# Performance work log

Measured on AMD Instinct MI355X. Metric: run time of the kernel, lower is better.

## Reference

```python
import jax, jax.numpy as jnp
import numpy as np

N, E, G = 50000, 400000, 2000
H, HEADS, HD = 128, 4, 32


def setup_inputs() -> dict:
    key = jax.random.key(0)
    ks = jax.random.split(key, 16)
    nrm = lambda k, shape, s=0.05: jax.random.normal(k, shape, dtype=jnp.float32) * s
    inp = {}
    inp["x"] = jax.random.normal(ks[0], (N, 39), dtype=jnp.float32)
    inp["edge_index"] = jax.random.randint(ks[1], (2, E), 0, N, dtype=jnp.int32)
    inp["edge_attr"] = jax.random.normal(ks[2], (E, 8), dtype=jnp.float32)
    inp["batch"] = jnp.sort(jax.random.randint(ks[3], (N,), 0, G, dtype=jnp.int32))
    inp["in_W"] = nrm(ks[4], (39, H)); inp["in_b"] = jnp.zeros((H,), jnp.float32)
    inp["in_g"] = jnp.ones((H,), jnp.float32); inp["in_beta"] = jnp.zeros((H,), jnp.float32)
    inp["Wl"] = nrm(ks[5], (3, H, H)); inp["Wr"] = nrm(ks[6], (3, H, H))
    inp["We"] = nrm(ks[7], (3, 8, H)); inp["att"] = nrm(ks[8], (3, HEADS, HD))
    inp["conv_b"] = jnp.zeros((3, H), jnp.float32)
    inp["bn_g"] = jnp.ones((3, H), jnp.float32); inp["bn_b"] = jnp.zeros((3, H), jnp.float32)
    inp["t1_W"] = nrm(ks[9], (3 * H, 256)); inp["t1_b"] = jnp.zeros((256,), jnp.float32)
    inp["t1_g"] = jnp.ones((256,), jnp.float32); inp["t1_beta"] = jnp.zeros((256,), jnp.float32)
    inp["t2_W"] = nrm(ks[10], (256, 128)); inp["t2_b"] = jnp.zeros((128,), jnp.float32)
    inp["t2_g"] = jnp.ones((128,), jnp.float32); inp["t2_beta"] = jnp.zeros((128,), jnp.float32)
    inp["head_W"] = nrm(ks[11], (128, 12)); inp["head_b"] = jnp.zeros((12,), jnp.float32)
    return inp


def _bn(h, g, b):
    # BatchNorm1d in training mode: normalize with batch statistics.
    m = h.mean(0)
    v = ((h - m) ** 2).mean(0)
    return g * (h - m) * jax.lax.rsqrt(v + 1e-5) + b


def reference(x, edge_index, edge_attr, batch, in_W, in_b, in_g, in_beta,
              Wl, Wr, We, att, conv_b, bn_g, bn_b,
              t1_W, t1_b, t1_g, t1_beta, t2_W, t2_b, t2_g, t2_beta,
              head_W, head_b):
    src, dst = edge_index[0], edge_index[1]  # messages flow src -> dst (PyG convention)
    xn = jax.nn.relu(_bn(x @ in_W + in_b, in_g, in_beta))  # [N, H]
    for l in range(3):  # three residual GATv2 layers
        xl = (xn @ Wl[l]).reshape(N, HEADS, HD)  # lin_l (source transform)
        xr = (xn @ Wr[l]).reshape(N, HEADS, HD)  # lin_r (target transform)
        ep = (edge_attr @ We[l]).reshape(E, HEADS, HD)
        m = jax.nn.leaky_relu(xl[src] + xr[dst] + ep, 0.2)  # [E, HEADS, HD]
        alpha = jnp.einsum('ehd,hd->eh', m, att[l])  # [E, HEADS]
        amax = jax.ops.segment_max(alpha, dst, num_segments=N)
        amax = jnp.where(jnp.isfinite(amax), amax, 0.0)  # nodes with no in-edges
        ae = jnp.exp(alpha - amax[dst])
        denom = jax.ops.segment_sum(ae, dst, num_segments=N)
        a = ae / (denom[dst] + 1e-16)  # scatter-softmax over neighborhoods
        agg = jax.ops.segment_sum(xl[src] * a[:, :, None], dst, num_segments=N)
        h = agg.reshape(N, H) + conv_b[l]
        h = jax.nn.elu(_bn(h, bn_g[l], bn_b[l]))
        xn = xn + h
    # 3-way global pooling per graph
    cnt = jax.ops.segment_sum(jnp.ones((N,), jnp.float32), batch, num_segments=G)
    sadd = jax.ops.segment_sum(xn, batch, num_segments=G)
    smean = sadd / jnp.maximum(cnt, 1.0)[:, None]
    smax = jax.ops.segment_max(xn, batch, num_segments=G)
    smax = jnp.where(cnt[:, None] > 0, smax, 0.0)
    xg = jnp.concatenate([smean, smax, sadd], axis=1)  # [G, 3H]
    t = jax.nn.relu(_bn(xg @ t1_W + t1_b, t1_g, t1_beta))
    t = jax.nn.relu(_bn(t @ t2_W + t2_b, t2_g, t2_beta))
    return jax.nn.sigmoid(t @ head_W + head_b)  # [G, 12]
```

## Files before the change

### kernel.cpp

```cpp
#include <hip/hip_runtime.h>
#include <math.h>


constexpr int N_ = 50000;
constexpr int E_ = 400000;
constexpr int G_ = 2000;
constexpr int H_ = 128;
constexpr int IN_ = 39;

typedef __attribute__((ext_vector_type(8))) short bf16x8;
typedef __attribute__((ext_vector_type(4))) float f32x4;

__device__ __forceinline__ unsigned pk_bf16(float a, float b) {
  unsigned ua = __float_as_uint(a);
  unsigned ub = __float_as_uint(b);
  ua = (ua + 0x7fffu + ((ua >> 16) & 1u)) >> 16;
  ub = (ub + 0x7fffu + ((ub >> 16) & 1u)) & 0xffff0000u;
  return ua | ub;
}
__device__ __forceinline__ unsigned short bf16_1(float x) {
  unsigned u = __float_as_uint(x);
  u = (u + 0x7fffu + ((u >> 16) & 1u)) >> 16;
  return (unsigned short)u;
}
__device__ __forceinline__ float up_lo(unsigned u) { return __uint_as_float(u << 16); }
__device__ __forceinline__ float up_hi(unsigned u) { return __uint_as_float(u & 0xffff0000u); }

template <int CTRL>
__device__ __forceinline__ float dpp_radd(float x) {
  int y = __builtin_amdgcn_update_dpp(0, __float_as_int(x), CTRL, 0xF, 0xF, false);
  return x + __int_as_float(y);
}
__device__ __forceinline__ float row_reduce16(float p) {
  p = dpp_radd<0x121>(p);
  p = dpp_radd<0x122>(p);
  p = dpp_radd<0x124>(p);
  p = dpp_radd<0x128>(p);
  return p;
}

__global__ __launch_bounds__(256) void hist_kernel(const int* __restrict__ keys, int n,
                                                   int* __restrict__ cnt) {
  for (int i = blockIdx.x * 256 + threadIdx.x; i < n; i += gridDim.x * 256)
    atomicAdd(&cnt[keys[i]], 1);
}

__global__ __launch_bounds__(1024) void scan_local(const int* __restrict__ in,
                                                   int* __restrict__ outx,
                                                   int* __restrict__ bsum, int n) {
  __shared__ int wsum[16];
  int t = threadIdx.x, lane = t & 63, wid = t >> 6;
  int idx = blockIdx.x * 1024 + t;
  int v = (idx < n) ? in[idx] : 0;
  int x = v;
#pragma unroll
  for (int off = 1; off < 64; off <<= 1) {
    int y = __shfl_up(x, off, 64);
    if (lane >= off) x += y;
  }
  if (lane == 63) wsum[wid] = x;
  __syncthreads();
  if (t == 0) {
    int acc = 0;
#pragma unroll
    for (int w = 0; w < 16; w++) { int tmp = wsum[w]; wsum[w] = acc; acc += tmp; }
    bsum[blockIdx.x] = acc;
  }
  __syncthreads();
  if (idx < n) outx[idx] = wsum[wid] + x - v;
}

__global__ __launch_bounds__(64) void scan_bsum(const int* __restrict__ bsum,
                                                int* __restrict__ boff, int nb) {
  int t = threadIdx.x;
  int v = (t < nb) ? bsum[t] : 0;
  int x = v;
#pragma unroll
  for (int off = 1; off < 64; off <<= 1) {
    int y = __shfl_up(x, off, 64);
    if (t >= off) x += y;
  }
  boff[t] = x - v;
}

__global__ __launch_bounds__(1024) void scan_add(int* __restrict__ eoff,
                                                 const int* __restrict__ boff,
                                                 int* __restrict__ cursor, int n) {
  int idx = blockIdx.x * 1024 + threadIdx.x;
  if (idx < n) {
    int e = eoff[idx] + boff[idx >> 10];
    eoff[idx] = e;
    cursor[idx] = e;
  }
  if (idx == 0) eoff[n] = E_;
}

__global__ __launch_bounds__(256) void goff_from_sorted(const int* __restrict__ batch,
                                                        int* __restrict__ goff) {
  int i = blockIdx.x * 256 + threadIdx.x;
  if (i >= N_) return;
  int bi = batch[i];
  int bp = (i == 0) ? -1 : batch[i - 1];
  for (int g = bp + 1; g <= bi; g++) goff[g] = i;
  if (i == N_ - 1) {
    for (int g = bi + 1; g <= G_; g++) goff[g] = N_;
  }
}

__global__ __launch_bounds__(256) void edge_scatter(const int* __restrict__ ei,
                                                    const float* __restrict__ ea,
                                                    int* __restrict__ cursor,
                                                    int* __restrict__ esrc,
                                                    unsigned* __restrict__ easb) {
  int e = blockIdx.x * 256 + threadIdx.x;
  if (e >= E_) return;
  int src = ei[e];
  int dst = ei[E_ + e];
  int j = atomicAdd(&cursor[dst], 1);
  esrc[j] = src;
  const float4* eav = (const float4*)(ea + (size_t)e * 8);
  float4 a0 = eav[0], a1 = eav[1];
  uint4 o;
  o.x = pk_bf16(a0.x, a0.y);
  o.y = pk_bf16(a0.z, a0.w);
  o.z = pk_bf16(a1.x, a1.y);
  o.w = pk_bf16(a1.z, a1.w);
  ((uint4*)easb)[j] = o;
}

__global__ __launch_bounds__(256) void pack_weights(const float* __restrict__ Wl,
                                                    const float* __restrict__ Wr,
                                                    unsigned short* __restrict__ wpack) {
  int i = blockIdx.x * 256 + threadIdx.x;
  if (i >= 3 * 128 * 256) return;
  int l = i >> 15;
  int rem = i & 32767;
  int k = rem >> 8;
  int n = rem & 255;
  const float* Wsrc = (n < 128) ? (Wl + l * H_ * H_) : (Wr + l * H_ * H_);
  int nn = n & 127;
  wpack[(size_t)l * 32768 + n * 128 + k] = bf16_1(Wsrc[k * H_ + nn]);
}

__global__ __launch_bounds__(256) void in_gemm(const float* __restrict__ x,
                                               const float* __restrict__ W,
                                               const float* __restrict__ b,
                                               float* __restrict__ y,
                                               float* __restrict__ ssum,
                                               float* __restrict__ ssq) {
  __shared__ float xs[32][40];
  __shared__ float s1[256], s2[256];
  int t = threadIdx.x;
  int row0 = blockIdx.x * 32;
  for (int i = t; i < 32 * IN_; i += 256) {
    int r = i / IN_, k = i % IN_;
    int row = row0 + r;
    xs[r][k] = (row < N_) ? x[row * IN_ + k] : 0.f;
  }
  __syncthreads();
  int col = t & 127;
  int half = t >> 7;
  float acc[16];
#pragma unroll
  for (int r = 0; r < 16; r++) acc[r] = 0.f;
  for (int k = 0; k < IN_; k++) {
    float w = W[k * H_ + col];
#pragma unroll
    for (int r = 0; r < 16; r++) acc[r] = fmaf(xs[half * 16 + r][k], w, acc[r]);
  }
  float bb = b[col];
  float a1 = 0.f, a2 = 0.f;
#pragma unroll
  for (int r = 0; r < 16; r++) {
    int row = row0 + half * 16 + r;
    float v = acc[r] + bb;
    if (row < N_) {
      y[row * H_ + col] = v;
      a1 += v;
      a2 = fmaf(v, v, a2);
    }
  }
  s1[t] = a1; s2[t] = a2;
  __syncthreads();
  if (t < 128) {
    atomicAdd(&ssum[t], s1[t] + s1[t + 128]);
    atomicAdd(&ssq[t], s2[t] + s2[t + 128]);
  }
}

template <int MODE>
__global__ __launch_bounds__(256) void gemm_mfma(float* __restrict__ xn,
                                                 const float* __restrict__ buf,
                                                 const float* __restrict__ g,
                                                 const float* __restrict__ beta,
                                                 const float* __restrict__ ssum,
                                                 const float* __restrict__ ssq,
                                                 float rows_inv,
                                                 const unsigned short* __restrict__ wp,
                                                 unsigned* __restrict__ xlb,
                                                 unsigned* __restrict__ xrb) {
  __shared__ char smem[17408 + 20480];
  short (*a_s)[136] = (short(*)[136])smem;
  short (*b_s)[40] = (short(*)[40])(smem + 17408);
  float* t2base = (float*)(smem + 17408);
  int t = threadIdx.x;
  int lane = t & 63, w = t >> 6;
  int quad = lane >> 4, lc = lane & 15;
  int row0 = blockIdx.x * 64;

  {
    int r = t >> 2;
    int row = row0 + r;
    int kb0 = (t & 3) * 32;
    bool valid = row < N_;
    for (int kk = 0; kk < 32; kk += 4) {
      int c = kb0 + kk;
      float4 v = make_float4(0.f, 0.f, 0.f, 0.f);
      if (valid) {
        float4 bv = *(const float4*)&buf[(size_t)row * H_ + c];
        float4 gv = *(const float4*)&g[c];
        float4 be = *(const float4*)&beta[c];
        float4 s1 = *(const float4*)&ssum[c];
        float4 s2 = *(const float4*)&ssq[c];
        float m0 = s1.x * rows_inv, m1 = s1.y * rows_inv, m2 = s1.z * rows_inv, m3 = s1.w * rows_inv;
        float r0 = rsqrtf(s2.x * rows_inv - m0 * m0 + 1e-5f);
        float r1 = rsqrtf(s2.y * rows_inv - m1 * m1 + 1e-5f);
        float r2 = rsqrtf(s2.z * rows_inv - m2 * m2 + 1e-5f);
        float r3 = rsqrtf(s2.w * rows_inv - m3 * m3 + 1e-5f);
        float t0 = gv.x * (bv.x - m0) * r0 + be.x;
        float t1 = gv.y * (bv.y - m1) * r1 + be.y;
        float t2 = gv.z * (bv.z - m2) * r2 + be.z;
        float t3 = gv.w * (bv.w - m3) * r3 + be.w;
        if (MODE == 1) {
          v = make_float4(fmaxf(t0, 0.f), fmaxf(t1, 0.f), fmaxf(t2, 0.f), fmaxf(t3, 0.f));
        } else {
          float4 xo = *(const float4*)&xn[(size_t)row * H_ + c];
          v.x = xo.x + ((t0 > 0.f) ? t0 : (__expf(t0) - 1.f));
          v.y = xo.y + ((t1 > 0.f) ? t1 : (__expf(t1) - 1.f));
          v.z = xo.z + ((t2 > 0.f) ? t2 : (__expf(t2) - 1.f));
          v.w = xo.w + ((t3 > 0.f) ? t3 : (__expf(t3) - 1.f));
        }
        *(float4*)&xn[(size_t)row * H_ + c] = v;
      }
      uint2 pk;
      pk.x = pk_bf16(v.x, v.y);
      pk.y = pk_bf16(v.z, v.w);
      *(uint2*)&a_s[r][c] = pk;
    }
  }

  f32x4 acc[16];
#pragma unroll
  for (int nt = 0; nt < 16; nt++) acc[nt] = (f32x4){0.f, 0.f, 0.f, 0.f};

  for (int kb = 0; kb < 4; kb++) {
    __syncthreads();
    for (int i = t; i < 1024; i += 256) {
      int n = i >> 2;
      int k8 = (i & 3) * 8;
      *(uint4*)&b_s[n][k8] = *(const uint4*)&wp[(size_t)n * 128 + kb * 32 + k8];
    }
    __syncthreads();
    bf16x8 av = *(const bf16x8*)&a_s[w * 16 + lc][kb * 32 + quad * 8];
#pragma unroll
    for (int nt = 0; nt < 16; nt++) {
      bf16x8 bv = *(const bf16x8*)&b_s[nt * 16 + lc][quad * 8];
      acc[nt] = __builtin_amdgcn_mfma_f32_16x16x32_bf16(av, bv, acc[nt], 0, 0, 0);
    }
  }
  __syncthreads();

  float* t2 = t2base + w * 544;
  for (int ntp = 0; ntp < 8; ntp++) {
#pragma unroll
    for (int rr = 0; rr < 4; rr++) {
      t2[(quad * 4 + rr) * 34 + lc] = acc[2 * ntp][rr];
      t2[(quad * 4 + rr) * 34 + 16 + lc] = acc[2 * ntp + 1][rr];
    }
    __asm__ volatile("s_waitcnt lgkmcnt(0)" ::: "memory");
#pragma unroll
    for (int it = 0; it < 4; it++) {
      int item = lane + it * 64;
      int p = item & 15, rowi = item >> 4;
      float v0 = t2[rowi * 34 + 2 * p];
      float v1 = t2[rowi * 34 + 2 * p + 1];
      unsigned u = pk_bf16(v0, v1);
      int colpair = ntp * 16 + p;
      int rowg = row0 + w * 16 + rowi;
      if (rowg < N_) {
        if (colpair < 64) xlb[(size_t)rowg * 64 + colpair] = u;
        else xrb[(size_t)rowg * 64 + colpair - 64] = u;
      }
    }
    __asm__ volatile("s_waitcnt lgkmcnt(0)" ::: "memory");
  }
}

__device__ __forceinline__ float ep8u(const uint4& u, const float* w) {
  float ep = up_lo(u.x) * w[0];
  ep = fmaf(up_hi(u.x), w[1], ep);
  ep = fmaf(up_lo(u.y), w[2], ep);
  ep = fmaf(up_hi(u.y), w[3], ep);
  ep = fmaf(up_lo(u.z), w[4], ep);
  ep = fmaf(up_hi(u.z), w[5], ep);
  ep = fmaf(up_lo(u.w), w[6], ep);
  ep = fmaf(up_hi(u.w), w[7], ep);
  return ep;
}

template <bool MASK>
__device__ __forceinline__ void pack4(int spre, int j, int cnt, int base, int l,
                                      const unsigned* __restrict__ xlb,
                                      const uint4* __restrict__ eas4,
                                      float xr0, float xr1,
                                      const float* w0, const float* w1,
                                      float2 attv,
                                      float& acc0, float& acc1, float& den) {
  int i0 = j;
  int i1 = j + 1, i2 = j + 2, i3 = j + 3;
  if (MASK) {
    i1 = (i1 < cnt) ? i1 : cnt - 1;
    i2 = (i2 < cnt) ? i2 : cnt - 1;
    i3 = (i3 < cnt) ? i3 : cnt - 1;
  }
  int s0 = __builtin_amdgcn_readlane(spre, i0);
  int s1 = __builtin_amdgcn_readlane(spre, i1);
  int s2 = __builtin_amdgcn_readlane(spre, i2);
  int s3 = __builtin_amdgcn_readlane(spre, i3);
  unsigned xu0 = xlb[(size_t)s0 * 64 + l];
  unsigned xu1 = xlb[(size_t)s1 * 64 + l];
  unsigned xu2 = xlb[(size_t)s2 * 64 + l];
  unsigned xu3 = xlb[(size_t)s3 * 64 + l];
  uint4 u0 = eas4[base + i0];
  uint4 u1 = eas4[base + i1];
  uint4 u2 = eas4[base + i2];
  uint4 u3 = eas4[base + i3];
  float x00 = up_lo(xu0), x01 = up_hi(xu0);
  float x10 = up_lo(xu1), x11 = up_hi(xu1);
  float x20 = up_lo(xu2), x21 = up_hi(xu2);
  float x30 = up_lo(xu3), x31 = up_hi(xu3);
  float m00 = x00 + xr0 + ep8u(u0, w0);
  float m01 = x01 + xr1 + ep8u(u0, w1);
  float m10 = x10 + xr0 + ep8u(u1, w0);
  float m11 = x11 + xr1 + ep8u(u1, w1);
  float m20 = x20 + xr0 + ep8u(u2, w0);
  float m21 = x21 + xr1 + ep8u(u2, w1);
  float m30 = x30 + xr0 + ep8u(u3, w0);
  float m31 = x31 + xr1 + ep8u(u3, w1);
  m00 = (m00 > 0.f) ? m00 : 0.2f * m00;
  m01 = (m01 > 0.f) ? m01 : 0.2f * m01;
  m10 = (m10 > 0.f) ? m10 : 0.2f * m10;
  m11 = (m11 > 0.f) ? m11 : 0.2f * m11;
  m20 = (m20 > 0.f) ? m20 : 0.2f * m20;
  m21 = (m21 > 0.f) ? m21 : 0.2f * m21;
  m30 = (m30 > 0.f) ? m30 : 0.2f * m30;
  m31 = (m31 > 0.f) ? m31 : 0.2f * m31;
  float p0 = fmaf(m00, attv.x, m01 * attv.y);
  float p1 = fmaf(m10, attv.x, m11 * attv.y);
  float p2 = fmaf(m20, attv.x, m21 * attv.y);
  float p3 = fmaf(m30, attv.x, m31 * attv.y);
  p0 = row_reduce16(p0);
  p1 = row_reduce16(p1);
  p2 = row_reduce16(p2);
  p3 = row_reduce16(p3);
  float e0v = __expf(p0), e1v = __expf(p1), e2v = __expf(p2), e3v = __expf(p3);
  if (MASK) {
    if (j + 1 >= cnt) e1v = 0.f;
    if (j + 2 >= cnt) e2v = 0.f;
    if (j + 3 >= cnt) e3v = 0.f;
  }
  acc0 = fmaf(e0v, x00, acc0); acc1 = fmaf(e0v, x01, acc1);
  acc0 = fmaf(e1v, x10, acc0); acc1 = fmaf(e1v, x11, acc1);
  acc0 = fmaf(e2v, x20, acc0); acc1 = fmaf(e2v, x21, acc1);
  acc0 = fmaf(e3v, x30, acc0); acc1 = fmaf(e3v, x31, acc1);
  den += (e0v + e1v) + (e2v + e3v);
}

__global__ __launch_bounds__(256) void agg_csr(const int* __restrict__ eoff,
                                               const int* __restrict__ esrc,
                                               const unsigned* __restrict__ easb,
                                               const float* __restrict__ Wel,
                                               const float* __restrict__ attl,
                                               const unsigned* __restrict__ xlb,
                                               const unsigned* __restrict__ xrb,
                                               const float* __restrict__ cb,
                                               float* __restrict__ buf,
                                               float* __restrict__ ssum,
                                               float* __restrict__ ssq) {
  __shared__ float sA[256], sB[256], sC[256], sD[256];
  int t = threadIdx.x;
  int l = t & 63;
  int sub = t >> 6;
  int c0 = l * 2;
  float w0[8], w1[8];
#pragma unroll
  for (int k = 0; k < 8; k++) {
    float2 wv = *(const float2*)&Wel[k * H_ + c0];
    w0[k] = wv.x; w1[k] = wv.y;
  }
  float2 attv = *(const float2*)&attl[c0];
  float2 cbv = *(const float2*)&cb[c0];
  const uint4* eas4 = (const uint4*)easb;
  float a1_0 = 0.f, a1_1 = 0.f, a2_0 = 0.f, a2_1 = 0.f;
  for (int n = blockIdx.x * 4 + sub; n < N_; n += gridDim.x * 4) {
    unsigned xru = xrb[(size_t)n * 64 + l];
    float xr0 = up_lo(xru), xr1 = up_hi(xru);
    int e0 = eoff[n], e1 = eoff[n + 1];
    float acc0 = 0.f, acc1 = 0.f, den = 0.f;
    for (int base = e0; base < e1; base += 64) {
      int cnt = min(64, e1 - base);
      int spre = (base + l < e1) ? esrc[base + l] : 0;
      int j = 0;
      for (; j + 4 <= cnt; j += 4)
        pack4<false>(spre, j, cnt, base, l, xlb, eas4, xr0, xr1, w0, w1, attv,
                     acc0, acc1, den);
      if (j < cnt)
        pack4<true>(spre, j, cnt, base, l, xlb, eas4, xr0, xr1, w0, w1, attv,
                    acc0, acc1, den);
    }
    float inv = 1.f / (den + 1e-16f);
    float h0 = acc0 * inv + cbv.x;
    float h1 = acc1 * inv + cbv.y;
    *(float2*)&buf[(size_t)n * H_ + c0] = make_float2(h0, h1);
    a1_0 += h0; a1_1 += h1;
    a2_0 = fmaf(h0, h0, a2_0); a2_1 = fmaf(h1, h1, a2_1);
  }
  sA[t] = a1_0; sB[t] = a1_1; sC[t] = a2_0; sD[t] = a2_1;
  __syncthreads();
  if (t < 64) {
    float r1 = sA[t] + sA[t + 64] + sA[t + 128] + sA[t + 192];
    float r2 = sB[t] + sB[t + 64] + sB[t + 128] + sB[t + 192];
    float r3 = sC[t] + sC[t + 64] + sC[t + 128] + sC[t + 192];
    float r4 = sD[t] + sD[t + 64] + sD[t + 128] + sD[t + 192];
    atomicAdd(&ssum[2 * t], r1);
    atomicAdd(&ssum[2 * t + 1], r2);
    atomicAdd(&ssq[2 * t], r3);
    atomicAdd(&ssq[2 * t + 1], r4);
  }
}

__global__ __launch_bounds__(256) void apply_bn_relu(const float* __restrict__ y,
                                                     float* __restrict__ out,
                                                     const float* __restrict__ g,
                                                     const float* __restrict__ beta,
                                                     const float* __restrict__ ssum,
                                                     const float* __restrict__ ssq,
                                                     float rows_inv,
                                                     long total, int cmask) {
  long i = (long)blockIdx.x * 256 + threadIdx.x;
  if (i >= total) return;
  int c = (int)i & cmask;
  float m = ssum[c] * rows_inv;
  float rs = rsqrtf(ssq[c] * rows_inv - m * m + 1e-5f);
  float v = g[c] * (y[i] - m) * rs + beta[c];
  out[i] = fmaxf(v, 0.f);
}

__global__ __launch_bounds__(128) void pool_residual(const int* __restrict__ goff,
                                                     const float* __restrict__ xn,
                                                     const float* __restrict__ buf,
                                                     const float* __restrict__ g,
                                                     const float* __restrict__ beta,
                                                     const float* __restrict__ ssum,
                                                     const float* __restrict__ ssq,
                                                     float rows_inv,
                                                     float* __restrict__ xg) {
  int gr = blockIdx.x;
  int t = threadIdx.x;
  int n0 = goff[gr], n1 = goff[gr + 1];
  float mm = ssum[t] * rows_inv;
  float rr = rsqrtf(ssq[t] * rows_inv - mm * mm + 1e-5f);
  float gg = g[t], bb = beta[t];
  float s = 0.f, mx = -INFINITY;
  for (int n = n0; n < n1; n++) {
    float w = gg * (buf[(size_t)n * H_ + t] - mm) * rr + bb;
    w = (w > 0.f) ? w : (__expf(w) - 1.f);
    float v = xn[(size_t)n * H_ + t] + w;
    s += v;
    mx = fmaxf(mx, v);
  }
  float c = (float)(n1 - n0);
  xg[gr * 384 + t] = s / fmaxf(c, 1.f);
  xg[gr * 384 + 128 + t] = (c > 0.f) ? mx : 0.f;
  xg[gr * 384 + 256 + t] = s;
}

template <int K, int COLS>
__global__ void mlp_gemm(const float* __restrict__ A, const float* __restrict__ W,
                         const float* __restrict__ b, float* __restrict__ Y, int rows,
                         float* __restrict__ ssum, float* __restrict__ ssq) {
  __shared__ float xs[8][K];
  int t = threadIdx.x;
  int row0 = blockIdx.x * 8;
  for (int i = t; i < 8 * K; i += COLS) {
    int r = i / K, k = i % K;
    int row = row0 + r;
    xs[r][k] = (row < rows) ? A[row * K + k] : 0.f;
  }
  __syncthreads();
  float acc[8];
#pragma unroll
  for (int r = 0; r < 8; r++) acc[r] = 0.f;
  for (int k = 0; k < K; k++) {
    float w = W[k * COLS + t];
#pragma unroll
    for (int r = 0; r < 8; r++) acc[r] = fmaf(xs[r][k], w, acc[r]);
  }
  float bb = b[t];
  float a1 = 0.f, a2 = 0.f;
#pragma unroll
  for (int r = 0; r < 8; r++) {
    int row = row0 + r;
    if (row < rows) {
      float v = acc[r] + bb;
      Y[row * COLS + t] = v;
      a1 += v;
      a2 = fmaf(v, v, a2);
    }
  }
  atomicAdd(&ssum[t], a1);
  atomicAdd(&ssq[t], a2);
}

__global__ __launch_bounds__(64) void head_kernel(const float* __restrict__ u,
                                                  const float* __restrict__ W,
                                                  const float* __restrict__ b,
                                                  float* __restrict__ out) {
  __shared__ float row[128];
  int g = blockIdx.x;
  int t = threadIdx.x;
  row[t] = u[g * 128 + t];
  row[t + 64] = u[g * 128 + 64 + t];
  __syncthreads();
  if (t < 12) {
    float acc = b[t];
    for (int k = 0; k < 128; k++) acc = fmaf(row[k], W[k * 12 + t], acc);
    out[g * 12 + t] = 1.f / (1.f + expf(-acc));
  }
}

extern "C" void kernel_launch(void* const* d_in, const int* in_sizes, int n_in, void* d_out,
                              int out_size, void* d_ws, size_t ws_size, hipStream_t stream) {
  (void)in_sizes; (void)n_in; (void)out_size; (void)ws_size;
  const float* x       = (const float*)d_in[0];
  const int*   ei      = (const int*)d_in[1];
  const float* ea      = (const float*)d_in[2];
  const int*   batch   = (const int*)d_in[3];
  const float* in_W    = (const float*)d_in[4];
  const float* in_b    = (const float*)d_in[5];
  const float* in_g    = (const float*)d_in[6];
  const float* in_beta = (const float*)d_in[7];
  const float* Wl      = (const float*)d_in[8];
  const float* Wr      = (const float*)d_in[9];
  const float* We      = (const float*)d_in[10];
  const float* att     = (const float*)d_in[11];
  const float* conv_b  = (const float*)d_in[12];
  const float* bn_g    = (const float*)d_in[13];
  const float* bn_b    = (const float*)d_in[14];
  const float* t1_W    = (const float*)d_in[15];
  const float* t1_b    = (const float*)d_in[16];
  const float* t1_g    = (const float*)d_in[17];
  const float* t1_beta = (const float*)d_in[18];
  const float* t2_W    = (const float*)d_in[19];
  const float* t2_b    = (const float*)d_in[20];
  const float* t2_g    = (const float*)d_in[21];
  const float* t2_beta = (const float*)d_in[22];
  const float* head_W  = (const float*)d_in[23];
  const float* head_b  = (const float*)d_in[24];
  float* out = (float*)d_out;

  float* p = (float*)d_ws;
  float* xn    = p; p += N_ * H_;
  float* buf   = p; p += N_ * H_;
  float* sstat = p; p += 6 * 512;
  float* xg    = p; p += G_ * 384;
  float* u1    = p; p += G_ * 256;
  float* u2    = p; p += G_ * 128;
  unsigned* up = (unsigned*)p;
  unsigned* xlb  = up; up += (size_t)N_ * 64;
  unsigned* xrb  = up; up += (size_t)N_ * 64;
  unsigned* easb = up; up += (size_t)E_ * 4;
  unsigned short* wpack = (unsigned short*)up; up += 3 * 32768 / 2;
  int* ip = (int*)up;
  int* deg    = ip; ip += N_;
  int* eoff   = ip; ip += N_ + 1;
  int* cursor = ip; ip += N_;
  int* goff   = ip; ip += G_ + 1;
  int* esrc   = ip; ip += E_;
  int* bsum   = ip; ip += 64;
  int* boff   = ip; ip += 64;

#define SSUM(s) (sstat + (s) * 512)
#define SSQ(s)  (sstat + (s) * 512 + 256)

  hipMemsetAsync(deg, 0, (size_t)N_ * sizeof(int), stream);
  hipMemsetAsync(sstat, 0, 6 * 512 * sizeof(float), stream);
  hist_kernel<<<1024, 256, 0, stream>>>(ei + E_, E_, deg);
  scan_local<<<49, 1024, 0, stream>>>(deg, eoff, bsum, N_);
  scan_bsum<<<1, 64, 0, stream>>>(bsum, boff, 49);
  scan_add<<<49, 1024, 0, stream>>>(eoff, boff, cursor, N_);
  edge_scatter<<<(E_ + 255) / 256, 256, 0, stream>>>(ei, ea, cursor, esrc, easb);
  goff_from_sorted<<<(N_ + 255) / 256, 256, 0, stream>>>(batch, goff);
  pack_weights<<<384, 256, 0, stream>>>(Wl, Wr, wpack);

  in_gemm<<<(N_ + 31) / 32, 256, 0, stream>>>(x, in_W, in_b, buf, SSUM(0), SSQ(0));

  const float rnInv = 1.f / N_;
  for (int l = 0; l < 3; l++) {
    if (l == 0) {
      gemm_mfma<1><<<782, 256, 0, stream>>>(xn, buf, in_g, in_beta, SSUM(0), SSQ(0), rnInv,
                                            wpack + (size_t)l * 32768, xlb, xrb);
    } else {
      gemm_mfma<2><<<782, 256, 0, stream>>>(xn, buf, bn_g + (l - 1) * H_, bn_b + (l - 1) * H_,
                                            SSUM(l), SSQ(l), rnInv,
                                            wpack + (size_t)l * 32768, xlb, xrb);
    }
    agg_csr<<<2048, 256, 0, stream>>>(eoff, esrc, easb, We + l * 8 * H_, att + l * H_,
                                      xlb, xrb, conv_b + l * H_, buf, SSUM(l + 1), SSQ(l + 1));
  }

  pool_residual<<<G_, 128, 0, stream>>>(goff, xn, buf, bn_g + 2 * H_, bn_b + 2 * H_,
                                        SSUM(3), SSQ(3), rnInv, xg);

  const float rgInv = 1.f / G_;
  mlp_gemm<384, 256><<<G_ / 8, 256, 0, stream>>>(xg, t1_W, t1_b, u1, G_, SSUM(4), SSQ(4));
  apply_bn_relu<<<(G_ * 256 + 255) / 256, 256, 0, stream>>>(u1, u1, t1_g, t1_beta,
                                                            SSUM(4), SSQ(4), rgInv,
                                                            (long)G_ * 256, 255);

  mlp_gemm<256, 128><<<G_ / 8, 128, 0, stream>>>(u1, t2_W, t2_b, u2, G_, SSUM(5), SSQ(5));
  apply_bn_relu<<<(G_ * 128 + 255) / 256, 256, 0, stream>>>(u2, u2, t2_g, t2_beta,
                                                            SSUM(5), SSQ(5), rgInv,
                                                            (long)G_ * 128, 127);

  head_kernel<<<G_, 64, 0, stream>>>(u2, head_W, head_b, out);
#undef SSUM
#undef SSQ
}
```

Baseline: 852.2 us.

## Process node pairs per wave with LDS-staged edge attrs and prefetched gathers

The CSR aggregation kernel now handles two consecutive destination nodes per wavefront. When their combined in-degree fits in 64, it stages the edge attributes in LDS and software-pipelines the gathers of source features one 4-edge pack ahead. The goal is to amortize per-node setup, cut partially filled 64-edge chunks for low-degree nodes, and hide gather latency. It costs extra branching and registers, and pairs whose combined degree exceeds 64 fall back to the old per-node path.

```diff
diff --git a/kernel.cpp b/kernel.cpp
--- a/kernel.cpp
+++ b/kernel.cpp
@@ -376,6 +376,25 @@
   den += (e0v + e1v) + (e2v + e3v);
 }
 
+__device__ __forceinline__ void solo_node(int e0, int e1, int l,
+                                          const int* __restrict__ esrc,
+                                          const unsigned* __restrict__ xlb,
+                                          const uint4* __restrict__ eas4,
+                                          float xr0, float xr1,
+                                          const float* w0, const float* w1,
+                                          float2 attv,
+                                          float& acc0, float& acc1, float& den) {
+  for (int base = e0; base < e1; base += 64) {
+    int cnt = min(64, e1 - base);
+    int spre = (base + l < e1) ? esrc[base + l] : 0;
+    int j = 0;
+    for (; j + 4 <= cnt; j += 4)
+      pack4<false>(spre, j, cnt, base, l, xlb, eas4, xr0, xr1, w0, w1, attv, acc0, acc1, den);
+    if (j < cnt)
+      pack4<true>(spre, j, cnt, base, l, xlb, eas4, xr0, xr1, w0, w1, attv, acc0, acc1, den);
+  }
+}
+
 __global__ __launch_bounds__(256) void agg_csr(const int* __restrict__ eoff,
                                                const int* __restrict__ esrc,
                                                const unsigned* __restrict__ easb,
@@ -388,10 +407,12 @@
                                                float* __restrict__ ssum,
                                                float* __restrict__ ssq) {
   __shared__ float sA[256], sB[256], sC[256], sD[256];
+  __shared__ uint4 eaLds[4][64];
   int t = threadIdx.x;
   int l = t & 63;
   int sub = t >> 6;
   int c0 = l * 2;
+  uint4* eaW = &eaLds[sub][0];
   float w0[8], w1[8];
 #pragma unroll
   for (int k = 0; k < 8; k++) {
@@ -402,28 +423,127 @@
   float2 cbv = *(const float2*)&cb[c0];
   const uint4* eas4 = (const uint4*)easb;
   float a1_0 = 0.f, a1_1 = 0.f, a2_0 = 0.f, a2_1 = 0.f;
-  for (int n = blockIdx.x * 4 + sub; n < N_; n += gridDim.x * 4) {
-    unsigned xru = xrb[(size_t)n * 64 + l];
-    float xr0 = up_lo(xru), xr1 = up_hi(xru);
-    int e0 = eoff[n], e1 = eoff[n + 1];
-    float acc0 = 0.f, acc1 = 0.f, den = 0.f;
-    for (int base = e0; base < e1; base += 64) {
-      int cnt = min(64, e1 - base);
-      int spre = (base + l < e1) ? esrc[base + l] : 0;
-      int j = 0;
-      for (; j + 4 <= cnt; j += 4)
-        pack4<false>(spre, j, cnt, base, l, xlb, eas4, xr0, xr1, w0, w1, attv,
-                     acc0, acc1, den);
-      if (j < cnt)
-        pack4<true>(spre, j, cnt, base, l, xlb, eas4, xr0, xr1, w0, w1, attv,
-                    acc0, acc1, den);
-    }
-    float inv = 1.f / (den + 1e-16f);
-    float h0 = acc0 * inv + cbv.x;
-    float h1 = acc1 * inv + cbv.y;
-    *(float2*)&buf[(size_t)n * H_ + c0] = make_float2(h0, h1);
-    a1_0 += h0; a1_1 += h1;
-    a2_0 = fmaf(h0, h0, a2_0); a2_1 = fmaf(h1, h1, a2_1);
+
+  for (int pi = blockIdx.x * 4 + sub; pi < N_ / 2; pi += gridDim.x * 4) {
+    int nA = 2 * pi, nB = nA + 1;
+    int e0A = eoff[nA], e1A = eoff[nA + 1], e1B = eoff[nA + 2];
+    unsigned xruA = xrb[(size_t)nA * 64 + l];
+    unsigned xruB = xrb[(size_t)nB * 64 + l];
+    int cE = e1B - e0A;
+    float hA0, hA1, hB0, hB1;
+    if (cE <= 64) {
+      int cA = e1A - e0A, cB = e1B - e1A;
+      if (l < cE) eaW[l] = eas4[e0A + l];
+      int spre = (l < cE) ? esrc[e0A + l] : 0;
+      __asm__ volatile("s_waitcnt lgkmcnt(0)" ::: "memory");
+      int nPA = (cA + 3) >> 2;
+      int nP = nPA + ((cB + 3) >> 2);
+      float accA0 = 0.f, accA1 = 0.f, denA = 0.f;
+      float accB0 = 0.f, accB1 = 0.f, denB = 0.f;
+      unsigned xu0 = 0, xu1 = 0, xu2 = 0, xu3 = 0;
+      int i0 = 0, i1 = 0, i2 = 0, i3 = 0;
+      if (nP > 0) {
+        bool isA = 0 < nPA;
+        int off = isA ? 0 : cA;
+        int cnt = isA ? cA : cB;
+        int lim = off + cnt - 1;
+        i0 = off;
+        i1 = min(off + 1, lim); i2 = min(off + 2, lim); i3 = min(off + 3, lim);
+        xu0 = xlb[(size_t)__builtin_amdgcn_readlane(spre, i0) * 64 + l];
+        xu1 = xlb[(size_t)__builtin_amdgcn_readlane(spre, i1) * 64 + l];
+        xu2 = xlb[(size_t)__builtin_amdgcn_readlane(spre, i2) * 64 + l];
+        xu3 = xlb[(size_t)__builtin_amdgcn_readlane(spre, i3) * 64 + l];
+      }
+      for (int k = 0; k < nP; k++) {
+        unsigned t0 = xu0, t1 = xu1, t2 = xu2, t3 = xu3;
+        int ci0 = i0, ci1 = i1, ci2 = i2, ci3 = i3;
+        bool isA = k < nPA;
+        int j = isA ? 4 * k : 4 * (k - nPA);
+        int cnt = isA ? cA : cB;
+        if (k + 1 < nP) {
+          bool pA = (k + 1) < nPA;
+          int off2 = pA ? 0 : cA;
+          int cnt2 = pA ? cA : cB;
+          int j2 = pA ? 4 * (k + 1) : 4 * (k + 1 - nPA);
+          int b2 = off2 + j2;
+          int lim2 = off2 + cnt2 - 1;
+          i0 = b2;
+          i1 = min(b2 + 1, lim2); i2 = min(b2 + 2, lim2); i3 = min(b2 + 3, lim2);
+          xu0 = xlb[(size_t)__builtin_amdgcn_readlane(spre, i0) * 64 + l];
+          xu1 = xlb[(size_t)__builtin_amdgcn_readlane(spre, i1) * 64 + l];
+          xu2 = xlb[(size_t)__builtin_amdgcn_readlane(spre, i2) * 64 + l];
+          xu3 = xlb[(size_t)__builtin_amdgcn_readlane(spre, i3) * 64 + l];
+        }
+        uint4 u0 = eaW[ci0], u1 = eaW[ci1], u2 = eaW[ci2], u3 = eaW[ci3];
+        unsigned xrp = isA ? xruA : xruB;
+        float xr0 = up_lo(xrp), xr1 = up_hi(xrp);
+        float x00 = up_lo(t0), x01 = up_hi(t0);
+        float x10 = up_lo(t1), x11 = up_hi(t1);
+        float x20 = up_lo(t2), x21 = up_hi(t2);
+        float x30 = up_lo(t3), x31 = up_hi(t3);
+        float m00 = x00 + xr0 + ep8u(u0, w0);
+        float m01 = x01 + xr1 + ep8u(u0, w1);
+        float m10 = x10 + xr0 + ep8u(u1, w0);
+        float m11 = x11 + xr1 + ep8u(u1, w1);
+        float m20 = x20 + xr0 + ep8u(u2, w0);
+        float m21 = x21 + xr1 + ep8u(u2, w1);
+        float m30 = x30 + xr0 + ep8u(u3, w0);
+        float m31 = x31 + xr1 + ep8u(u3, w1);
+        m00 = (m00 > 0.f) ? m00 : 0.2f * m00;
+        m01 = (m01 > 0.f) ? m01 : 0.2f * m01;
+        m10 = (m10 > 0.f) ? m10 : 0.2f * m10;
+        m11 = (m11 > 0.f) ? m11 : 0.2f * m11;
+        m20 = (m20 > 0.f) ? m20 : 0.2f * m20;
+        m21 = (m21 > 0.f) ? m21 : 0.2f * m21;
+        m30 = (m30 > 0.f) ? m30 : 0.2f * m30;
+        m31 = (m31 > 0.f) ? m31 : 0.2f * m31;
+        float p0 = fmaf(m00, attv.x, m01 * attv.y);
+        float p1 = fmaf(m10, attv.x, m11 * attv.y);
+        float p2 = fmaf(m20, attv.x, m21 * attv.y);
+        float p3 = fmaf(m30, attv.x, m31 * attv.y);
+        p0 = row_reduce16(p0);
+        p1 = row_reduce16(p1);
+        p2 = row_reduce16(p2);
+        p3 = row_reduce16(p3);
+        float e0v = __expf(p0), e1v = __expf(p1), e2v = __expf(p2), e3v = __expf(p3);
+        if (j + 1 >= cnt) e1v = 0.f;
+        if (j + 2 >= cnt) e2v = 0.f;
+        if (j + 3 >= cnt) e3v = 0.f;
+        if (isA) {
+          accA0 = fmaf(e0v, x00, accA0); accA1 = fmaf(e0v, x01, accA1);
+          accA0 = fmaf(e1v, x10, accA0); accA1 = fmaf(e1v, x11, accA1);
+          accA0 = fmaf(e2v, x20, accA0); accA1 = fmaf(e2v, x21, accA1);
+          accA0 = fmaf(e3v, x30, accA0); accA1 = fmaf(e3v, x31, accA1);
+          denA += (e0v + e1v) + (e2v + e3v);
+        } else {
+          accB0 = fmaf(e0v, x00, accB0); accB1 = fmaf(e0v, x01, accB1);
+          accB0 = fmaf(e1v, x10, accB0); accB1 = fmaf(e1v, x11, accB1);
+          accB0 = fmaf(e2v, x20, accB0); accB1 = fmaf(e2v, x21, accB1);
+          accB0 = fmaf(e3v, x30, accB0); accB1 = fmaf(e3v, x31, accB1);
+          denB += (e0v + e1v) + (e2v + e3v);
+        }
+      }
+      float invA = 1.f / (denA + 1e-16f);
+      float invB = 1.f / (denB + 1e-16f);
+      hA0 = accA0 * invA + cbv.x; hA1 = accA1 * invA + cbv.y;
+      hB0 = accB0 * invB + cbv.x; hB1 = accB1 * invB + cbv.y;
+    } else {
+      float accA0 = 0.f, accA1 = 0.f, denA = 0.f;
+      float accB0 = 0.f, accB1 = 0.f, denB = 0.f;
+      solo_node(e0A, e1A, l, esrc, xlb, eas4, up_lo(xruA), up_hi(xruA),
+                w0, w1, attv, accA0, accA1, denA);
+      solo_node(e1A, e1B, l, esrc, xlb, eas4, up_lo(xruB), up_hi(xruB),
+                w0, w1, attv, accB0, accB1, denB);
+      float invA = 1.f / (denA + 1e-16f);
+      float invB = 1.f / (denB + 1e-16f);
+      hA0 = accA0 * invA + cbv.x; hA1 = accA1 * invA + cbv.y;
+      hB0 = accB0 * invB + cbv.x; hB1 = accB1 * invB + cbv.y;
+    }
+    *(float2*)&buf[(size_t)nA * H_ + c0] = make_float2(hA0, hA1);
+    *(float2*)&buf[(size_t)nB * H_ + c0] = make_float2(hB0, hB1);
+    a1_0 += hA0 + hB0; a1_1 += hA1 + hB1;
+    a2_0 = fmaf(hA0, hA0, a2_0); a2_0 = fmaf(hB0, hB0, a2_0);
+    a2_1 = fmaf(hA1, hA1, a2_1); a2_1 = fmaf(hB1, hB1, a2_1);
   }
   sA[t] = a1_0; sB[t] = a1_1; sC[t] = a2_0; sD[t] = a2_1;
   __syncthreads();
```

Result: no change. 841.4 us (-1.3%).
